# Performance work log

Measured on AMD Instinct MI355X. Metric: run time of the kernel, lower is better.

The kernel has to match this reference:

```python
import jax, jax.numpy as jnp
import numpy as np

R = 3                 # corr_radius
STRIDE = 4
RES = (384, 512)      # model_resolution (H, W)
G = 2 * R + 1         # 7: support grid side


def setup_inputs() -> dict:
    key = jax.random.key(0)
    ks = jax.random.split(key, 16)
    B, S, N, C = 1, 8, 1024, 128
    H0, W0 = RES[0] // STRIDE, RES[1] // STRIDE  # 96, 128
    inp = {}
    for i in range(4):
        h, w = H0 >> i, W0 >> i
        inp[f"fmaps{i}"] = jax.random.normal(ks[i], (B, S, C, h, w), jnp.float32)
        inp[f"track{i}"] = jax.random.normal(ks[4 + i], (B, G * G, N, C), jnp.float32)
    inp["coords"] = jax.random.uniform(ks[8], (B, S, N, 2), jnp.float32) * jnp.asarray([W0 - 1.0, H0 - 1.0], jnp.float32)
    inp["vis"] = jax.random.normal(ks[9], (B, S, N, 1), jnp.float32)
    inp["conf"] = jax.random.normal(ks[10], (B, S, N, 1), jnp.float32)
    r2 = G * G
    inp["w1"] = jax.random.normal(ks[11], (r2 * r2, 384), jnp.float32) * (1.0 / np.sqrt(r2 * r2))
    inp["b1"] = jnp.zeros((384,), jnp.float32)
    inp["w2"] = jax.random.normal(ks[12], (384, 256), jnp.float32) * (1.0 / np.sqrt(384))
    inp["b2"] = jnp.zeros((256,), jnp.float32)
    inp["time_emb"] = jax.random.normal(ks[13], (1, S, 1110), jnp.float32) * 0.02
    return inp


def bilinear_sample(fmap, x, y):
    """fmap: (BT, C, H, W); x, y: (BT, M) pixel coords. Border padding, align_corners=True
    (matches torch grid_sample as used by co-tracker's bilinear_sampler)."""
    BT, C, H, W = fmap.shape
    x0f = jnp.floor(x)
    y0f = jnp.floor(y)
    wx = (x - x0f)[:, None, :]
    wy = (y - y0f)[:, None, :]
    x0 = jnp.clip(x0f.astype(jnp.int32), 0, W - 1)
    x1 = jnp.clip(x0f.astype(jnp.int32) + 1, 0, W - 1)
    y0 = jnp.clip(y0f.astype(jnp.int32), 0, H - 1)
    y1 = jnp.clip(y0f.astype(jnp.int32) + 1, 0, H - 1)
    flat = fmap.reshape(BT, C, H * W)

    def g(yi, xi):
        idx = (yi * W + xi)[:, None, :]  # (BT, 1, M)
        return jnp.take_along_axis(flat, idx, axis=2)  # (BT, C, M)

    return (g(y0, x0) * (1 - wx) * (1 - wy) + g(y0, x1) * wx * (1 - wy)
            + g(y1, x0) * (1 - wx) * wy + g(y1, x1) * wx * wy)


def posenc(x, min_deg=0, max_deg=10):
    scales = jnp.asarray([2.0 ** i for i in range(min_deg, max_deg)], x.dtype)
    xb = (x[..., None, :] * scales[:, None]).reshape(x.shape[:-1] + (-1,))
    four = jnp.sin(jnp.concatenate([xb, xb + 0.5 * jnp.pi], axis=-1))
    return jnp.concatenate([x, four], axis=-1)


def reference(fmaps0, fmaps1, fmaps2, fmaps3, track0, track1, track2, track3,
              coords, vis, conf, w1, b1, w2, b2, time_emb):
    B, S, N, _ = coords.shape
    fps = [fmaps0, fmaps1, fmaps2, fmaps3]
    tps = [track0, track1, track2, track3]
    d = jnp.linspace(-R, R, G)
    xoff, yoff = jnp.meshgrid(d, d, indexing='ij')  # (7,7): rows = x offset, cols = y offset

    embs = []
    for lvl in range(4):
        fm = fps[lvl]
        C, H, W = fm.shape[2], fm.shape[3], fm.shape[4]
        c = coords.reshape(B * S, N, 1, 1, 2) / (2.0 ** lvl)
        x = c[..., 0] + xoff          # (B*S, N, 7, 7)
        y = c[..., 1] + yoff
        M = N * G * G
        sampled = bilinear_sample(fm.reshape(B * S, C, H, W), x.reshape(B * S, M), y.reshape(B * S, M))
        corr_feat = sampled.reshape(B, S, C, N, G, G).transpose(0, 1, 3, 4, 5, 2)  # (B,S,N,7,7,C)
        track = tps[lvl].reshape(B, G, G, N, C).transpose(0, 3, 1, 2, 4)           # (B,N,7,7,C)
        vol = jnp.einsum('btnhwc,bnijc->btnhwij', corr_feat, track)                # (B,S,N,7,7,7,7)
        h = jax.nn.gelu(vol.reshape(B * S * N, G * G * G * G) @ w1 + b1, approximate=False)
        embs.append(h @ w2 + b2)
    corr_embs = jnp.concatenate(embs, axis=-1).reshape(B, S, N, -1)  # (B,S,N,1024)

    rel_f = jnp.pad(coords[:, :-1] - coords[:, 1:], ((0, 0), (0, 1), (0, 0), (0, 0)))
    rel_b = jnp.pad(coords[:, 1:] - coords[:, :-1], ((0, 0), (1, 0), (0, 0), (0, 0)))
    scale = jnp.asarray([RES[1], RES[0]], jnp.float32) / STRIDE
    rel_emb = posenc(jnp.concatenate([rel_f / scale, rel_b / scale], axis=-1))  # (B,S,N,84)

    x = jnp.concatenate([vis, conf, corr_embs, rel_emb], axis=-1)  # (B,S,N,1110)
    x = x.transpose(0, 2, 1, 3).reshape(B * N, S, -1) + time_emb
    return x.reshape(B, N, S, -1)
```

## Files before the change

### kernel.cpp

```cpp
#include <hip/hip_runtime.h>
#include <math.h>


#define SN 8
#define NN 1024
#define CC 128
#define K1P 2432
#define H1 384
#define H2 256
#define DOUT 1110

typedef short bf16x8 __attribute__((ext_vector_type(8)));
typedef float f32x4 __attribute__((ext_vector_type(4)));

__device__ inline unsigned short f2b(float x) {
    union { float f; unsigned u; } v; v.f = x;
    unsigned r = v.u + 0x7FFFu + ((v.u >> 16) & 1u);
    return (unsigned short)(r >> 16);
}
__device__ inline float b2f(unsigned short u) {
    union { unsigned u; float f; } v; v.u = (unsigned)u << 16; return v.f;
}
__device__ inline void gll16(const void* g, void* l) {
    __builtin_amdgcn_global_load_lds(
        (const __attribute__((address_space(1))) void*)g,
        (__attribute__((address_space(3))) void*)l, 16, 0, 0);
}
__device__ inline int swz(int row, int g) {
    return row * 128 + ((g ^ (row & 7)) << 3);
}

__global__ __launch_bounds__(256) void conv_fmap_kernel(
    const float* __restrict__ in, unsigned short* __restrict__ outp,
    int H, int W)
{
    const int Hp = H + 8, Wp = W + 8;
    const int s = blockIdx.x / Hp, yp = blockIdx.x % Hp;
    const int y = min(max(yp - 4, 0), H - 1);
    const float* src = in + (size_t)s * CC * H * W + (size_t)y * W;
    unsigned short* dst = outp + ((size_t)s * Hp + yp) * Wp * CC;
    for (int idx = threadIdx.x; idx < Wp * CC; idx += 256) {
        int xp = idx >> 7, c = idx & 127;
        int x = min(max(xp - 4, 0), W - 1);
        dst[idx] = f2b(src[(size_t)c * H * W + x]);
    }
}

__global__ __launch_bounds__(256, 3) void sample_vol_kernel(
    const unsigned short* __restrict__ fq0, const unsigned short* __restrict__ fq1,
    const unsigned short* __restrict__ fq2, const unsigned short* __restrict__ fq3,
    const float* __restrict__ tk0, const float* __restrict__ tk1,
    const float* __restrict__ tk2, const float* __restrict__ tk3,
    const float* __restrict__ coords,
    unsigned short* __restrict__ vol,
    int lv0)
{
    __shared__ __align__(16) unsigned short patch[80 * 128];
    __shared__ __align__(16) unsigned short trk[64 * 128];
    __shared__ __align__(16) unsigned short pcL[80 * 66];
    const int n = blockIdx.x & 1023, g = blockIdx.x >> 10;
    const int lvl = lv0 + g;
    const unsigned short* fpad = (lvl == 0) ? fq0 : (lvl == 1) ? fq1
                               : (lvl == 2) ? fq2 : fq3;
    const float* track = (lvl == 0) ? tk0 : (lvl == 1) ? tk1
                       : (lvl == 2) ? tk2 : tk3;
    const int Wp = (128 >> lvl) + 8;
    const int t = threadIdx.x;
    const int lane = t & 63, wv = t >> 6;
    const int rsub = lane & 15, kq = lane >> 4;
    const float inv = 1.0f / (float)(1 << lvl);
    const size_t plane = (size_t)((96 >> lvl) + 8) * Wp * CC;

    int poff[5], ldso[5];
    #pragma unroll
    for (int i = 0; i < 5; ++i) {
        int task64 = wv * 5 + i;
        int point = task64 * 4 + (lane >> 4);
        int v = point / 10, xs = point - v * 10;
        int j = (lane & 15) ^ (point & 7);
        poff[i] = (v * Wp + xs) * CC + j * 8;
        ldso[i] = task64 * 512;
    }

    float cxa[SN], cya[SN];
    #pragma unroll
    for (int s = 0; s < SN; ++s) {
        float2 c2 = *(const float2*)&coords[((size_t)s * NN + n) * 2];
        cxa[s] = c2.x * inv; cya[s] = c2.y * inv;
    }

    unsigned lutA[5], lutB[5];
    #pragma unroll
    for (int i = 0; i < 5; ++i) {
        int d = t + i * 256;
        int o0 = 2 * d, o1 = 2 * d + 1;
        lutA[i] = 0xFFFFFFFFu; lutB[i] = 0xFFFFFFFFu;
        if (o0 < 2401) {
            int ab = o0 / 49, ij = o0 - 49 * ab, a = ab / 7, b = ab - 7 * a;
            lutA[i] = (unsigned)((b * 10 + a) * 66 + ij);
        }
        if (o1 < 2401) {
            int ab = o1 / 49, ij = o1 - 49 * ab, a = ab / 7, b = ab - 7 * a;
            lutB[i] = (unsigned)((b * 10 + a) * 66 + ij);
        }
    }

    int fx = (int)floorf(cxa[0]), fy = (int)floorf(cya[0]);
    int e = (fx - 3) & ~1;
    {
        const unsigned short* base = fpad + ((fy + 1) * Wp + (e + 4)) * CC;
        #pragma unroll
        for (int i = 0; i < 5; ++i) gll16(base + poff[i], &patch[ldso[i]]);
    }
    for (int task = t; task < 49 * 16; task += 256) {
        int row = task >> 4, gg = task & 15;
        const float* srcp = &track[((size_t)row * NN + n) * CC + gg * 8];
        float4 f0 = *(const float4*)srcp;
        float4 f1 = *(const float4*)(srcp + 4);
        bf16x8 v8;
        v8[0] = f2b(f0.x); v8[1] = f2b(f0.y); v8[2] = f2b(f0.z); v8[3] = f2b(f0.w);
        v8[4] = f2b(f1.x); v8[5] = f2b(f1.y); v8[6] = f2b(f1.z); v8[7] = f2b(f1.w);
        *(bf16x8*)&trk[swz(row, gg)] = v8;
    }

    #pragma unroll
    for (int sl = 0; sl < SN; ++sl) {
        const float wx = cxa[sl] - (float)fx, wy = cya[sl] - (float)fy;
        const float w00 = (1.f - wx) * (1.f - wy), w10 = wx * (1.f - wy);
        const float w01 = (1.f - wx) * wy,         w11 = wx * wy;
        const int offs = (fx - 3 - e) * 66;

        if (sl == 0)      asm volatile("s_waitcnt vmcnt(0) lgkmcnt(0)" ::: "memory");
        else if (wv == 3) asm volatile("s_waitcnt vmcnt(4) lgkmcnt(0)" ::: "memory");
        else              asm volatile("s_waitcnt vmcnt(5) lgkmcnt(0)" ::: "memory");
        __builtin_amdgcn_sched_barrier(0);
        __builtin_amdgcn_s_barrier();
        __builtin_amdgcn_sched_barrier(0);

        {
            f32x4 acc[5] = {};
            #pragma unroll
            for (int kk = 0; kk < 4; ++kk) {
                int gg = kk * 4 + kq;
                bf16x8 b = *(const bf16x8*)&trk[swz(wv * 16 + rsub, gg)];
                #pragma unroll
                for (int ti = 0; ti < 5; ++ti) {
                    bf16x8 a = *(const bf16x8*)&patch[swz(ti * 16 + rsub, gg)];
                    acc[ti] = __builtin_amdgcn_mfma_f32_16x16x32_bf16(a, b, acc[ti], 0, 0, 0);
                }
            }
            const int col = wv * 16 + rsub;
            #pragma unroll
            for (int ti = 0; ti < 5; ++ti)
                #pragma unroll
                for (int r = 0; r < 4; ++r)
                    pcL[(ti * 16 + kq * 4 + r) * 66 + col] = f2b(acc[ti][r]);
        }
        asm volatile("s_waitcnt lgkmcnt(0)" ::: "memory");
        __builtin_amdgcn_s_barrier();
        __builtin_amdgcn_sched_barrier(0);

        if (sl + 1 < SN) {
            fx = (int)floorf(cxa[sl + 1]); fy = (int)floorf(cya[sl + 1]);
            e = (fx - 3) & ~1;
            const unsigned short* base =
                fpad + (size_t)(sl + 1) * plane + ((fy + 1) * Wp + (e + 4)) * CC;
            #pragma unroll
            for (int i = 0; i < 5; ++i) gll16(base + poff[i], &patch[ldso[i]]);
        }
        __builtin_amdgcn_sched_barrier(0);

        {
            unsigned* vrow32 = (unsigned*)(vol + ((size_t)(g * SN + sl) * NN + n) * K1P);
            #pragma unroll
            for (int i = 0; i < 5; ++i) {
                int d = t + i * 256;
                if (d < K1P / 2) {
                    unsigned lo = 0, hi = 0;
                    if (lutA[i] != 0xFFFFFFFFu) {
                        int idx = (int)lutA[i] + offs;
                        float v = w00 * b2f(pcL[idx])       + w10 * b2f(pcL[idx + 66])
                                + w01 * b2f(pcL[idx + 660]) + w11 * b2f(pcL[idx + 726]);
                        lo = f2b(v);
                    }
                    if (lutB[i] != 0xFFFFFFFFu) {
                        int idx = (int)lutB[i] + offs;
                        float v = w00 * b2f(pcL[idx])       + w10 * b2f(pcL[idx + 66])
                                + w01 * b2f(pcL[idx + 660]) + w11 * b2f(pcL[idx + 726]);
                        hi = f2b(v);
                    }
                    vrow32[d] = lo | (hi << 16);
                }
            }
        }
    }
}

__global__ __launch_bounds__(256, 3) void gemm1_kernel(
    const unsigned short* __restrict__ A,
    const unsigned short* __restrict__ Bt,
    const float* __restrict__ bias,
    unsigned short* __restrict__ Hout)
{
    __shared__ __align__(16) unsigned short As[3 * 128 * 32];
    __shared__ __align__(16) unsigned short Bs[3 * 128 * 32];
    const int h = blockIdx.x, q = gridDim.x >> 3;
    const int l = (h & 7) * q + (h >> 3);
    const int m0 = (l / 3) * 128, n0 = (l % 3) * 128;
    const int t = threadIdx.x, lane = t & 63, wv = t >> 6;
    const int wm = wv >> 1, wn = wv & 1;
    const int rsub = lane & 15, kq = lane >> 4;

    const int rA0 = t >> 2, sA0 = (t & 3) ^ ((rA0 >> 1) & 3);
    const int rA1 = (t + 256) >> 2, sA1 = ((t + 256) & 3) ^ ((rA1 >> 1) & 3);
    const unsigned short* gA0 = A  + (size_t)(m0 + rA0) * K1P + sA0 * 8;
    const unsigned short* gA1 = A  + (size_t)(m0 + rA1) * K1P + sA1 * 8;
    const unsigned short* gB0 = Bt + (size_t)(n0 + rA0) * K1P + sA0 * 8;
    const unsigned short* gB1 = Bt + (size_t)(n0 + rA1) * K1P + sA1 * 8;
    const int chunk0 = (t & ~63) * 8, chunk1 = (256 + (t & ~63)) * 8;

    f32x4 acc[4][4] = {};

    const int NSTEP = K1P / 32;
    #pragma unroll
    for (int p = 0; p < 3; ++p) {
        size_t ko = (size_t)p * 32;
        int lb = p * 4096;
        gll16(gA0 + ko, &As[lb + chunk0]); gll16(gA1 + ko, &As[lb + chunk1]);
        gll16(gB0 + ko, &Bs[lb + chunk0]); gll16(gB1 + ko, &Bs[lb + chunk1]);
    }
    int cur = 0;
    for (int st = 0; st < NSTEP; ++st) {
        const int rem = NSTEP - 1 - st;
        if (rem >= 2)      asm volatile("s_waitcnt vmcnt(8)" ::: "memory");
        else if (rem == 1) asm volatile("s_waitcnt vmcnt(4)" ::: "memory");
        else               asm volatile("s_waitcnt vmcnt(0)" ::: "memory");
        __builtin_amdgcn_s_barrier();
        __builtin_amdgcn_sched_barrier(0);
        const int lb = cur * 4096;
        bf16x8 af[4], bfr[4];
        #pragma unroll
        for (int mi = 0; mi < 4; ++mi) {
            int r = wm * 64 + mi * 16 + rsub;
            int phys = r * 4 + (kq ^ ((r >> 1) & 3));
            af[mi] = *(const bf16x8*)&As[lb + phys * 8];
        }
        #pragma unroll
        for (int ni = 0; ni < 4; ++ni) {
            int r = wn * 64 + ni * 16 + rsub;
            int phys = r * 4 + (kq ^ ((r >> 1) & 3));
            bfr[ni] = *(const bf16x8*)&Bs[lb + phys * 8];
        }
        #pragma unroll
        for (int mi = 0; mi < 4; ++mi)
            #pragma unroll
            for (int ni = 0; ni < 4; ++ni)
                acc[mi][ni] = __builtin_amdgcn_mfma_f32_16x16x32_bf16(
                    af[mi], bfr[ni], acc[mi][ni], 0, 0, 0);
        __builtin_amdgcn_sched_barrier(0);
        __builtin_amdgcn_s_barrier();
        __builtin_amdgcn_sched_barrier(0);
        if (st + 3 < NSTEP) {
            size_t ko = (size_t)(st + 3) * 32;
            gll16(gA0 + ko, &As[lb + chunk0]);
            gll16(gA1 + ko, &As[lb + chunk1]);
            gll16(gB0 + ko, &Bs[lb + chunk0]);
            gll16(gB1 + ko, &Bs[lb + chunk1]);
        }
        cur = (cur == 2) ? 0 : cur + 1;
    }
    #pragma unroll
    for (int mi = 0; mi < 4; ++mi) {
        int row = m0 + wm * 64 + mi * 16 + kq * 4;
        #pragma unroll
        for (int ni = 0; ni < 4; ++ni) {
            int col = n0 + wn * 64 + ni * 16 + rsub;
            float bcol = bias[col];
            #pragma unroll
            for (int r = 0; r < 4; ++r) {
                float x = acc[mi][ni][r] + bcol;
                float gg = 0.5f * x * (1.f + erff(x * 0.70710678118654752f));
                Hout[(size_t)(row + r) * H1 + col] = f2b(gg);
            }
        }
    }
}

__global__ __launch_bounds__(256, 3) void gemm2_kernel(
    const unsigned short* __restrict__ A,
    const unsigned short* __restrict__ Bt,
    const float* __restrict__ bias,
    const float* __restrict__ te,
    float* __restrict__ out,
    int lv0)
{
    __shared__ __align__(16) unsigned short As[3 * 128 * 32];
    __shared__ __align__(16) unsigned short Bs[3 * 128 * 32];
    const int h = blockIdx.x, q = gridDim.x >> 3;
    const int l = (h & 7) * q + (h >> 3);
    const int m0 = (l >> 1) * 128, n0 = (l & 1) * 128;
    const int t = threadIdx.x, lane = t & 63, wv = t >> 6;
    const int wm = wv >> 1, wn = wv & 1;
    const int rsub = lane & 15, kq = lane >> 4;

    const int rA0 = t >> 2, sA0 = (t & 3) ^ ((rA0 >> 1) & 3);
    const int rA1 = (t + 256) >> 2, sA1 = ((t + 256) & 3) ^ ((rA1 >> 1) & 3);
    const unsigned short* gA0 = A  + (size_t)(m0 + rA0) * H1 + sA0 * 8;
    const unsigned short* gA1 = A  + (size_t)(m0 + rA1) * H1 + sA1 * 8;
    const unsigned short* gB0 = Bt + (size_t)(n0 + rA0) * H1 + sA0 * 8;
    const unsigned short* gB1 = Bt + (size_t)(n0 + rA1) * H1 + sA1 * 8;
    const int chunk0 = (t & ~63) * 8, chunk1 = (256 + (t & ~63)) * 8;

    f32x4 acc[4][4] = {};

    const int NSTEP = H1 / 32;
    #pragma unroll
    for (int p = 0; p < 3; ++p) {
        size_t ko = (size_t)p * 32;
        int lb = p * 4096;
        gll16(gA0 + ko, &As[lb + chunk0]); gll16(gA1 + ko, &As[lb + chunk1]);
        gll16(gB0 + ko, &Bs[lb + chunk0]); gll16(gB1 + ko, &Bs[lb + chunk1]);
    }
    int cur = 0;
    for (int st = 0; st < NSTEP; ++st) {
        const int rem = NSTEP - 1 - st;
        if (rem >= 2)      asm volatile("s_waitcnt vmcnt(8)" ::: "memory");
        else if (rem == 1) asm volatile("s_waitcnt vmcnt(4)" ::: "memory");
        else               asm volatile("s_waitcnt vmcnt(0)" ::: "memory");
        __builtin_amdgcn_s_barrier();
        __builtin_amdgcn_sched_barrier(0);
        const int lb = cur * 4096;
        bf16x8 af[4], bfr[4];
        #pragma unroll
        for (int mi = 0; mi < 4; ++mi) {
            int r = wm * 64 + mi * 16 + rsub;
            int phys = r * 4 + (kq ^ ((r >> 1) & 3));
            af[mi] = *(const bf16x8*)&As[lb + phys * 8];
        }
        #pragma unroll
        for (int ni = 0; ni < 4; ++ni) {
            int r = wn * 64 + ni * 16 + rsub;
            int phys = r * 4 + (kq ^ ((r >> 1) & 3));
            bfr[ni] = *(const bf16x8*)&Bs[lb + phys * 8];
        }
        #pragma unroll
        for (int mi = 0; mi < 4; ++mi)
            #pragma unroll
            for (int ni = 0; ni < 4; ++ni)
                acc[mi][ni] = __builtin_amdgcn_mfma_f32_16x16x32_bf16(
                    af[mi], bfr[ni], acc[mi][ni], 0, 0, 0);
        __builtin_amdgcn_sched_barrier(0);
        __builtin_amdgcn_s_barrier();
        __builtin_amdgcn_sched_barrier(0);
        if (st + 3 < NSTEP) {
            size_t ko = (size_t)(st + 3) * 32;
            gll16(gA0 + ko, &As[lb + chunk0]);
            gll16(gA1 + ko, &As[lb + chunk1]);
            gll16(gB0 + ko, &Bs[lb + chunk0]);
            gll16(gB1 + ko, &Bs[lb + chunk1]);
        }
        cur = (cur == 2) ? 0 : cur + 1;
    }
    #pragma unroll
    for (int mi = 0; mi < 4; ++mi) {
        int rowb = m0 + wm * 64 + mi * 16 + kq * 4;
        #pragma unroll
        for (int ni = 0; ni < 4; ++ni) {
            int col = n0 + wn * 64 + ni * 16 + rsub;
            float bcol = bias[col];
            #pragma unroll
            for (int r = 0; r < 4; ++r) {
                int row = rowb + r;
                int g = row >> 13, s = (row >> 10) & 7, n = row & 1023;
                int dcol = 2 + (lv0 + g) * H2 + col;
                out[((size_t)n * SN + s) * DOUT + dcol] =
                    acc[mi][ni][r] + bcol + te[s * DOUT + dcol];
            }
        }
    }
}

__global__ __launch_bounds__(256) void conv_t_kernel(
    const float* __restrict__ in, unsigned short* __restrict__ outp,
    int K, int Nw, int Kp)
{
    __shared__ float tile[32][33];
    const int kb = blockIdx.x * 32, nb = blockIdx.y * 32;
    const int tx = threadIdx.x & 31, ty = threadIdx.x >> 5;
    #pragma unroll
    for (int i = 0; i < 32; i += 8) {
        int k = kb + ty + i, nn = nb + tx;
        tile[ty + i][tx] = (k < K && nn < Nw) ? in[(size_t)k * Nw + nn] : 0.f;
    }
    __syncthreads();
    #pragma unroll
    for (int i = 0; i < 32; i += 8) {
        int nn = nb + ty + i, k = kb + tx;
        if (nn < Nw) outp[(size_t)nn * Kp + k] = f2b(tile[tx][ty + i]);
    }
}

__global__ __launch_bounds__(128) void tail_kernel(
    const float* __restrict__ coords, const float* __restrict__ vis,
    const float* __restrict__ conf, const float* __restrict__ te,
    float* __restrict__ out)
{
    const int b = blockIdx.x;
    const int n = b >> 3, s = b & 7;
    const int d = threadIdx.x;
    if (d >= 86) return;
    const size_t ob = (size_t)b * DOUT;
    if (d == 0) {
        out[ob + 0] = vis[(size_t)s * NN + n] + te[s * DOUT + 0];
    } else if (d == 1) {
        out[ob + 1] = conf[(size_t)s * NN + n] + te[s * DOUT + 1];
    } else {
        int rd = d - 2;
        float cx = coords[((size_t)s * NN + n) * 2 + 0];
        float cy = coords[((size_t)s * NN + n) * 2 + 1];
        float rfx = 0.f, rfy = 0.f, rbx = 0.f, rby = 0.f;
        if (s < SN - 1) {
            rfx = cx - coords[((size_t)(s + 1) * NN + n) * 2 + 0];
            rfy = cy - coords[((size_t)(s + 1) * NN + n) * 2 + 1];
        }
        if (s > 0) {
            rbx = cx - coords[((size_t)(s - 1) * NN + n) * 2 + 0];
            rby = cy - coords[((size_t)(s - 1) * NN + n) * 2 + 1];
        }
        float r4[4] = {rfx / 128.f, rfy / 96.f, rbx / 128.f, rby / 96.f};
        float val;
        if (rd < 4) {
            val = r4[rd];
        } else if (rd < 44) {
            int q = rd - 4; int deg = q >> 2, comp = q & 3;
            val = sinf(r4[comp] * (float)(1 << deg));
        } else {
            int q = rd - 44; int deg = q >> 2, comp = q & 3;
            val = sinf(r4[comp] * (float)(1 << deg) + 1.57079632679489662f);
        }
        int od = 1026 + rd;
        out[ob + od] = val + te[s * DOUT + od];
    }
}

extern "C" void kernel_launch(void* const* d_in, const int* in_sizes, int n_in,
                              void* d_out, int out_size, void* d_ws, size_t ws_size,
                              hipStream_t stream) {
    const float* fmaps[4] = {(const float*)d_in[0], (const float*)d_in[2],
                             (const float*)d_in[4], (const float*)d_in[6]};
    const float* track[4] = {(const float*)d_in[1], (const float*)d_in[3],
                             (const float*)d_in[5], (const float*)d_in[7]};
    const float* coords = (const float*)d_in[8];
    const float* vis    = (const float*)d_in[9];
    const float* conf   = (const float*)d_in[10];
    const float* w1     = (const float*)d_in[11];
    const float* b1     = (const float*)d_in[12];
    const float* w2     = (const float*)d_in[13];
    const float* b2     = (const float*)d_in[14];
    const float* te     = (const float*)d_in[15];
    float* out = (float*)d_out;

    const int Hs[4] = {96, 48, 24, 12};
    const int Ws[4] = {128, 64, 32, 16};

    char* wsb = (char*)d_ws;
    unsigned short* w1t = (unsigned short*)wsb;
    size_t off = (size_t)H1 * K1P * 2;
    unsigned short* w2t = (unsigned short*)(wsb + off);
    off += (size_t)H2 * H1 * 2;
    unsigned short* fpad[4];
    for (int l = 0; l < 4; ++l) {
        fpad[l] = (unsigned short*)(wsb + off);
        off += (size_t)SN * (Hs[l] + 8) * (Ws[l] + 8) * CC * 2;
    }
    off += 512;
    const size_t fixed = off;
    int n_lv = 4;
    while (n_lv > 1 &&
           fixed + (size_t)n_lv * SN * NN * (K1P + H1) * 2 > ws_size)
        n_lv >>= 1;
    unsigned short* volb = (unsigned short*)(wsb + fixed);
    unsigned short* hb   = volb + (size_t)n_lv * SN * NN * K1P;

    conv_t_kernel<<<dim3(K1P / 32, H1 / 32), 256, 0, stream>>>(w1, w1t, 2401, H1, K1P);
    conv_t_kernel<<<dim3(H1 / 32, H2 / 32), 256, 0, stream>>>(w2, w2t, H1, H2, H1);
    for (int l = 0; l < 4; ++l)
        conv_fmap_kernel<<<SN * (Hs[l] + 8), 256, 0, stream>>>(
            fmaps[l], fpad[l], Hs[l], Ws[l]);

    for (int lv0 = 0; lv0 < 4; lv0 += n_lv) {
        sample_vol_kernel<<<n_lv * NN, 256, 0, stream>>>(
            fpad[0], fpad[1], fpad[2], fpad[3],
            track[0], track[1], track[2], track[3],
            coords, volb, lv0);
        const int rows = n_lv * SN * NN;
        gemm1_kernel<<<(rows / 128) * 3, 256, 0, stream>>>(volb, w1t, b1, hb);
        gemm2_kernel<<<(rows / 128) * 2, 256, 0, stream>>>(hb, w2t, b2, te, out, lv0);
    }
    tail_kernel<<<SN * NN, 128, 0, stream>>>(coords, vis, conf, te, out);
}
```

Baseline: 344.6 us.

## Pad correlation volume K to 8-aligned blocks for vectorized bilinear stores

Changes the volume layout so each 49-element inner block is padded to 56 (K grows from 2432 to 2752), with w1 reordered and zero-padded to match. Each thread now reads 8 contiguous correlation values per corner with vector LDS loads and writes 16-byte global stores, in place of scattered scalar gathers and 4-byte stores. Track fragments are also hoisted into registers once rather than reloaded every time step. The cost is a GEMM1 that is about 13% larger in K and more workspace, plus an extra zero-pad kernel.

```diff
diff --git a/kernel.cpp b/kernel.cpp
--- a/kernel.cpp
+++ b/kernel.cpp
@@ -5,12 +5,13 @@
 #define SN 8
 #define NN 1024
 #define CC 128
-#define K1P 2432
+#define K1P2 2752
 #define H1 384
 #define H2 256
 #define DOUT 1110
 
 typedef short bf16x8 __attribute__((ext_vector_type(8)));
+typedef short s16x4 __attribute__((ext_vector_type(4)));
 typedef float f32x4 __attribute__((ext_vector_type(4)));
 
 __device__ inline unsigned short f2b(float x) {
@@ -57,7 +58,7 @@
 {
     __shared__ __align__(16) unsigned short patch[80 * 128];
     __shared__ __align__(16) unsigned short trk[64 * 128];
-    __shared__ __align__(16) unsigned short pcL[80 * 66];
+    __shared__ __align__(16) unsigned short pcL[80 * 68];
     const int n = blockIdx.x & 1023, g = blockIdx.x >> 10;
     const int lvl = lv0 + g;
     const unsigned short* fpad = (lvl == 0) ? fq0 : (lvl == 1) ? fq1
@@ -89,20 +90,17 @@
         cxa[s] = c2.x * inv; cya[s] = c2.y * inv;
     }
 
-    unsigned lutA[5], lutB[5];
-    #pragma unroll
-    for (int i = 0; i < 5; ++i) {
-        int d = t + i * 256;
-        int o0 = 2 * d, o1 = 2 * d + 1;
-        lutA[i] = 0xFFFFFFFFu; lutB[i] = 0xFFFFFFFFu;
-        if (o0 < 2401) {
-            int ab = o0 / 49, ij = o0 - 49 * ab, a = ab / 7, b = ab - 7 * a;
-            lutA[i] = (unsigned)((b * 10 + a) * 66 + ij);
-        }
-        if (o1 < 2401) {
-            int ab = o1 / 49, ij = o1 - 49 * ab, a = ab / 7, b = ab - 7 * a;
-            lutB[i] = (unsigned)((b * 10 + a) * 66 + ij);
-        }
+    int p0b[2], ij0a[2], tau8[2]; bool vld[2];
+    #pragma unroll
+    for (int rep = 0; rep < 2; ++rep) {
+        int tau = t + rep * 256;
+        vld[rep] = (tau < 343);
+        int tt = vld[rep] ? tau : 0;
+        int ab = tt / 7, blk = tt - 7 * ab;
+        int a = ab / 7, b = ab - 7 * a;
+        p0b[rep] = b * 10 + a;
+        ij0a[rep] = blk * 8;
+        tau8[rep] = tt * 8;
     }
 
     int fx = (int)floorf(cxa[0]), fy = (int)floorf(cya[0]);
@@ -122,17 +120,27 @@
         v8[4] = f2b(f1.x); v8[5] = f2b(f1.y); v8[6] = f2b(f1.z); v8[7] = f2b(f1.w);
         *(bf16x8*)&trk[swz(row, gg)] = v8;
     }
+    {
+        unsigned* T32 = (unsigned*)trk;
+        for (int i = t; i < 15 * 64; i += 256) T32[49 * 64 + i] = 0;
+    }
+    asm volatile("s_waitcnt lgkmcnt(0)" ::: "memory");
+    __builtin_amdgcn_s_barrier();
+    bf16x8 tf[4];
+    #pragma unroll
+    for (int kk = 0; kk < 4; ++kk)
+        tf[kk] = *(const bf16x8*)&trk[swz(wv * 16 + rsub, kk * 4 + kq)];
 
     #pragma unroll
     for (int sl = 0; sl < SN; ++sl) {
         const float wx = cxa[sl] - (float)fx, wy = cya[sl] - (float)fy;
         const float w00 = (1.f - wx) * (1.f - wy), w10 = wx * (1.f - wy);
         const float w01 = (1.f - wx) * wy,         w11 = wx * wy;
-        const int offs = (fx - 3 - e) * 66;
-
-        if (sl == 0)      asm volatile("s_waitcnt vmcnt(0) lgkmcnt(0)" ::: "memory");
-        else if (wv == 3) asm volatile("s_waitcnt vmcnt(4) lgkmcnt(0)" ::: "memory");
-        else              asm volatile("s_waitcnt vmcnt(5) lgkmcnt(0)" ::: "memory");
+        const int off = fx - 3 - e;
+
+        if (sl == 0)     asm volatile("s_waitcnt vmcnt(0) lgkmcnt(0)" ::: "memory");
+        else if (wv < 2) asm volatile("s_waitcnt vmcnt(2) lgkmcnt(0)" ::: "memory");
+        else             asm volatile("s_waitcnt vmcnt(1) lgkmcnt(0)" ::: "memory");
         __builtin_amdgcn_sched_barrier(0);
         __builtin_amdgcn_s_barrier();
         __builtin_amdgcn_sched_barrier(0);
@@ -142,11 +150,10 @@
             #pragma unroll
             for (int kk = 0; kk < 4; ++kk) {
                 int gg = kk * 4 + kq;
-                bf16x8 b = *(const bf16x8*)&trk[swz(wv * 16 + rsub, gg)];
                 #pragma unroll
                 for (int ti = 0; ti < 5; ++ti) {
                     bf16x8 a = *(const bf16x8*)&patch[swz(ti * 16 + rsub, gg)];
-                    acc[ti] = __builtin_amdgcn_mfma_f32_16x16x32_bf16(a, b, acc[ti], 0, 0, 0);
+                    acc[ti] = __builtin_amdgcn_mfma_f32_16x16x32_bf16(a, tf[kk], acc[ti], 0, 0, 0);
                 }
             }
             const int col = wv * 16 + rsub;
@@ -154,7 +161,7 @@
             for (int ti = 0; ti < 5; ++ti)
                 #pragma unroll
                 for (int r = 0; r < 4; ++r)
-                    pcL[(ti * 16 + kq * 4 + r) * 66 + col] = f2b(acc[ti][r]);
+                    pcL[(ti * 16 + kq * 4 + r) * 68 + col] = f2b(acc[ti][r]);
         }
         asm volatile("s_waitcnt lgkmcnt(0)" ::: "memory");
         __builtin_amdgcn_s_barrier();
@@ -171,29 +178,69 @@
         __builtin_amdgcn_sched_barrier(0);
 
         {
-            unsigned* vrow32 = (unsigned*)(vol + ((size_t)(g * SN + sl) * NN + n) * K1P);
-            #pragma unroll
-            for (int i = 0; i < 5; ++i) {
-                int d = t + i * 256;
-                if (d < K1P / 2) {
-                    unsigned lo = 0, hi = 0;
-                    if (lutA[i] != 0xFFFFFFFFu) {
-                        int idx = (int)lutA[i] + offs;
-                        float v = w00 * b2f(pcL[idx])       + w10 * b2f(pcL[idx + 66])
-                                + w01 * b2f(pcL[idx + 660]) + w11 * b2f(pcL[idx + 726]);
-                        lo = f2b(v);
+            unsigned short* vrow = vol + ((size_t)(g * SN + sl) * NN + n) * K1P2;
+            #pragma unroll
+            for (int rep = 0; rep < 2; ++rep) {
+                if (vld[rep]) {
+                    int base = (p0b[rep] + off) * 68 + ij0a[rep];
+                    s16x4 a0 = *(const s16x4*)&pcL[base],       a1 = *(const s16x4*)&pcL[base + 4];
+                    s16x4 b0 = *(const s16x4*)&pcL[base + 68],  b1 = *(const s16x4*)&pcL[base + 72];
+                    s16x4 c0 = *(const s16x4*)&pcL[base + 680], c1 = *(const s16x4*)&pcL[base + 684];
+                    s16x4 d0 = *(const s16x4*)&pcL[base + 748], d1 = *(const s16x4*)&pcL[base + 752];
+                    unsigned w[4];
+                    #pragma unroll
+                    for (int j = 0; j < 4; ++j) {
+                        const int e0 = 2 * j, e1 = 2 * j + 1;
+                        float v0 = w00 * b2f((unsigned short)(e0 < 4 ? a0[e0 & 3] : a1[e0 & 3]))
+                                 + w10 * b2f((unsigned short)(e0 < 4 ? b0[e0 & 3] : b1[e0 & 3]))
+                                 + w01 * b2f((unsigned short)(e0 < 4 ? c0[e0 & 3] : c1[e0 & 3]))
+                                 + w11 * b2f((unsigned short)(e0 < 4 ? d0[e0 & 3] : d1[e0 & 3]));
+                        float v1 = w00 * b2f((unsigned short)(e1 < 4 ? a0[e1 & 3] : a1[e1 & 3]))
+                                 + w10 * b2f((unsigned short)(e1 < 4 ? b0[e1 & 3] : b1[e1 & 3]))
+                                 + w01 * b2f((unsigned short)(e1 < 4 ? c0[e1 & 3] : c1[e1 & 3]))
+                                 + w11 * b2f((unsigned short)(e1 < 4 ? d0[e1 & 3] : d1[e1 & 3]));
+                        w[j] = (unsigned)f2b(v0) | ((unsigned)f2b(v1) << 16);
                     }
-                    if (lutB[i] != 0xFFFFFFFFu) {
-                        int idx = (int)lutB[i] + offs;
-                        float v = w00 * b2f(pcL[idx])       + w10 * b2f(pcL[idx + 66])
-                                + w01 * b2f(pcL[idx + 660]) + w11 * b2f(pcL[idx + 726]);
-                        hi = f2b(v);
-                    }
-                    vrow32[d] = lo | (hi << 16);
+                    uint4 st; st.x = w[0]; st.y = w[1]; st.z = w[2]; st.w = w[3];
+                    *(uint4*)(vrow + tau8[rep]) = st;
                 }
             }
         }
     }
+}
+
+__global__ __launch_bounds__(256) void zpad_kernel(
+    unsigned short* __restrict__ vol, int rows)
+{
+    int r = blockIdx.x * 256 + threadIdx.x;
+    if (r < rows) {
+        uint4 z; z.x = 0; z.y = 0; z.z = 0; z.w = 0;
+        *(uint4*)(vol + (size_t)r * K1P2 + 2744) = z;
+    }
+}
+
+__global__ __launch_bounds__(256) void conv_w1_kernel(
+    const float* __restrict__ w1, unsigned short* __restrict__ w1t)
+{
+    __shared__ float tile[32][33];
+    const int kb = blockIdx.x * 32, nb = blockIdx.y * 32;
+    const int tx = threadIdx.x & 31, ty = threadIdx.x >> 5;
+    #pragma unroll
+    for (int i = 0; i < 32; i += 8) {
+        int kp = kb + ty + i;
+        int k = -1;
+        if (kp < 2744) {
+            int tau = kp >> 3, r = kp & 7;
+            int ab = tau / 7, blk = tau - 7 * ab;
+            int ij = blk * 8 + r;
+            if (ij < 49) k = ab * 49 + ij;
+        }
+        tile[ty + i][tx] = (k >= 0) ? w1[(size_t)k * H1 + nb + tx] : 0.f;
+    }
+    __syncthreads();
+    #pragma unroll
+    for (int i = 0; i < 32; i += 8)
+        w1t[(size_t)(nb + ty + i) * K1P2 + kb + tx] = f2b(tile[tx][ty + i]);
 }
 
 __global__ __launch_bounds__(256, 3) void gemm1_kernel(
@@ -213,15 +260,15 @@
 
     const int rA0 = t >> 2, sA0 = (t & 3) ^ ((rA0 >> 1) & 3);
     const int rA1 = (t + 256) >> 2, sA1 = ((t + 256) & 3) ^ ((rA1 >> 1) & 3);
-    const unsigned short* gA0 = A  + (size_t)(m0 + rA0) * K1P + sA0 * 8;
-    const unsigned short* gA1 = A  + (size_t)(m0 + rA1) * K1P + sA1 * 8;
-    const unsigned short* gB0 = Bt + (size_t)(n0 + rA0) * K1P + sA0 * 8;
-    const unsigned short* gB1 = Bt + (size_t)(n0 + rA1) * K1P + sA1 * 8;
+    const unsigned short* gA0 = A  + (size_t)(m0 + rA0) * K1P2 + sA0 * 8;
+    const unsigned short* gA1 = A  + (size_t)(m0 + rA1) * K1P2 + sA1 * 8;
+    const unsigned short* gB0 = Bt + (size_t)(n0 + rA0) * K1P2 + sA0 * 8;
+    const unsigned short* gB1 = Bt + (size_t)(n0 + rA1) * K1P2 + sA1 * 8;
     const int chunk0 = (t & ~63) * 8, chunk1 = (256 + (t & ~63)) * 8;
 
     f32x4 acc[4][4] = {};
 
-    const int NSTEP = K1P / 32;
+    const int NSTEP = K1P2 / 32;
     #pragma unroll
     for (int p = 0; p < 3; ++p) {
         size_t ko = (size_t)p * 32;
@@ -465,7 +512,7 @@
 
     char* wsb = (char*)d_ws;
     unsigned short* w1t = (unsigned short*)wsb;
-    size_t off = (size_t)H1 * K1P * 2;
+    size_t off = (size_t)H1 * K1P2 * 2;
     unsigned short* w2t = (unsigned short*)(wsb + off);
     off += (size_t)H2 * H1 * 2;
     unsigned short* fpad[4];
@@ -477,16 +524,18 @@
     const size_t fixed = off;
     int n_lv = 4;
     while (n_lv > 1 &&
-           fixed + (size_t)n_lv * SN * NN * (K1P + H1) * 2 > ws_size)
+           fixed + (size_t)n_lv * SN * NN * (K1P2 + H1) * 2 > ws_size)
         n_lv >>= 1;
     unsigned short* volb = (unsigned short*)(wsb + fixed);
-    unsigned short* hb   = volb + (size_t)n_lv * SN * NN * K1P;
-
-    conv_t_kernel<<<dim3(K1P / 32, H1 / 32), 256, 0, stream>>>(w1, w1t, 2401, H1, K1P);
+    unsigned short* hb   = volb + (size_t)n_lv * SN * NN * K1P2;
+
+    conv_w1_kernel<<<dim3(K1P2 / 32, H1 / 32), 256, 0, stream>>>(w1, w1t);
     conv_t_kernel<<<dim3(H1 / 32, H2 / 32), 256, 0, stream>>>(w2, w2t, H1, H2, H1);
     for (int l = 0; l < 4; ++l)
         conv_fmap_kernel<<<SN * (Hs[l] + 8), 256, 0, stream>>>(
             fmaps[l], fpad[l], Hs[l], Ws[l]);
+    zpad_kernel<<<(n_lv * SN * NN + 255) / 256, 256, 0, stream>>>(
+        volb, n_lv * SN * NN);
 
     for (int lv0 = 0; lv0 < 4; lv0 += n_lv) {
         sample_vol_kernel<<<n_lv * NN, 256, 0, stream>>>(
```

Result: no change. 346.0 us (+0.4%).
